# Optimization experiments

Measured on AMD Instinct MI355X. Metric: run time of the kernel, lower is better.

## Reference

```python
import jax, jax.numpy as jnp
import numpy as np
from jax import lax

B, L, P, CIN, N, HD, PH, K = 2048, 96, 96, 8, 64, 64, 8, 3
DIM_C = CIN * N  # 512


def _silu(x):
    return x * jax.nn.sigmoid(x)


def _lin(x, w, b):
    return x @ w.T + b


def setup_inputs() -> dict:
    key = jax.random.key(0)
    ks = iter(jax.random.split(key, 64))

    def w(shape):
        fan_in = shape[-1]
        return (jax.random.normal(next(ks), shape, jnp.float32) / np.sqrt(fan_in)).astype(jnp.float32)

    inp = {"x": jax.random.normal(next(ks), (B, L, CIN), jnp.float32)}
    # x_proj: 5 Linears (enc_in->h, h->h, h->h, h->h, h->N), SiLU between (dropout=eval/identity)
    inp["xp_w0"] = w((HD, CIN)); inp["xp_b0"] = jnp.zeros((HD,), jnp.float32)
    inp["xp_w1"] = w((HD, HD));  inp["xp_b1"] = jnp.zeros((HD,), jnp.float32)
    inp["xp_w2"] = w((HD, HD));  inp["xp_b2"] = jnp.zeros((HD,), jnp.float32)
    inp["xp_w3"] = w((HD, HD));  inp["xp_b3"] = jnp.zeros((HD,), jnp.float32)
    inp["xp_w4"] = w((N, HD));   inp["xp_b4"] = jnp.zeros((N,), jnp.float32)
    # x_proj_: Linear(N,h), SiLU, Linear(h,N)
    inp["xpp_w0"] = w((HD, N)); inp["xpp_b0"] = jnp.zeros((HD,), jnp.float32)
    inp["xpp_w1"] = w((N, HD)); inp["xpp_b1"] = jnp.zeros((N,), jnp.float32)
    # depthwise dilated Conv1d: weight (N, 1, K)
    inp["conv_w"] = w((N, 1, K)); inp["conv_b"] = jnp.zeros((N,), jnp.float32)
    inp["span_A"] = jnp.asarray(0.1, jnp.float32)
    # compress: Linear(N*L, PH)
    inp["comp_w"] = w((PH, N * L)); inp["comp_b"] = jnp.zeros((PH,), jnp.float32)
    # a_ode.net: Linear(PH,h), SiLU, Linear(h,PH), Tanh
    inp["net_w0"] = w((HD, PH)); inp["net_b0"] = jnp.zeros((HD,), jnp.float32)
    inp["net_w1"] = w((PH, HD)); inp["net_b1"] = jnp.zeros((PH,), jnp.float32)
    # lat2out: Linear(PH,8), SiLU, Linear(8,N)
    inp["lo_w0"] = w((8, PH)); inp["lo_b0"] = jnp.zeros((8,), jnp.float32)
    inp["lo_w1"] = w((N, 8));  inp["lo_b1"] = jnp.zeros((N,), jnp.float32)
    # lat2out_c: Linear(PH,8), SiLU, Linear(8, CIN*N)
    inp["lc_w0"] = w((8, PH));     inp["lc_b0"] = jnp.zeros((8,), jnp.float32)
    inp["lc_w1"] = w((DIM_C, 8));  inp["lc_b1"] = jnp.zeros((DIM_C,), jnp.float32)
    # lat2out_z: Linear(N,N), SiLU, Linear(N, CIN)
    inp["lz_w0"] = w((N, N));   inp["lz_b0"] = jnp.zeros((N,), jnp.float32)
    inp["lz_w1"] = w((CIN, N)); inp["lz_b1"] = jnp.zeros((CIN,), jnp.float32)
    return inp


def reference(x, xp_w0, xp_b0, xp_w1, xp_b1, xp_w2, xp_b2, xp_w3, xp_b3, xp_w4, xp_b4,
              xpp_w0, xpp_b0, xpp_w1, xpp_b1, conv_w, conv_b, span_A, comp_w, comp_b,
              net_w0, net_b0, net_w1, net_b1, lo_w0, lo_b0, lo_w1, lo_b1,
              lc_w0, lc_b0, lc_w1, lc_b1, lz_w0, lz_b0, lz_w1, lz_b1):
    Bsz = x.shape[0]

    def x_proj(t):
        h = _silu(_lin(t, xp_w0, xp_b0))
        h = _silu(_lin(h, xp_w1, xp_b1))
        h = _silu(_lin(h, xp_w2, xp_b2))
        h = _silu(_lin(h, xp_w3, xp_b3))
        return _lin(h, xp_w4, xp_b4)

    x_old = x_proj(x[:, :L])                       # (B, L, N)
    hist = x_old.transpose(0, 2, 1)                # (B, N, L)
    pad = (K - 1) * 2                              # 4
    conv = lax.conv_general_dilated(
        hist, conv_w, window_strides=(1,), padding=[(pad, pad)],
        rhs_dilation=(2,), dimension_numbers=("NCH", "OIH", "NCH"),
        feature_group_count=N) + conv_b[None, :, None]
    hist = _silu(conv)[:, :, -L:]                  # (B, N, L)
    hist_f = hist.transpose(0, 2, 1).reshape(Bsz, L * N)
    vector_F = _lin(hist_f, comp_w, comp_b)        # (B, PH)

    a0 = vector_F
    z0 = x_proj(x[:, L - 1])                       # (B, N)

    # Householder matrix H = I - 2 v v^T with v = normalize(x_proj_(z0))
    v = _lin(_silu(_lin(z0, xpp_w0, xpp_b0)), xpp_w1, xpp_b1)
    v = v / (jnp.linalg.norm(v, axis=-1, keepdims=True) + 1e-8)
    Hh = jnp.eye(N, dtype=x.dtype)[None] - 2.0 * v[:, :, None] * v[:, None, :]  # (B,N,N)

    dt = jnp.clip(span_A, 1e-8, 7.0)               # uniform Euler step size
    s0 = jnp.concatenate([a0, z0], axis=-1)        # (B, PH+N)

    def step(s, _):
        a = s[:, :PH]
        z = s[:, PH:]
        da = jnp.tanh(_lin(_silu(_lin(a, net_w0, net_b0)), net_w1, net_b1))  # (B,PH)
        d = _lin(_silu(_lin(a, lo_w0, lo_b0)), lo_w1, lo_b1)                 # (B,N)
        # dz = H^T diag(d) H z   (fused; avoids materializing A_mat)
        Hz = jnp.einsum('bjk,bk->bj', Hh, z)
        dz = jnp.einsum('bj,bji->bi', d * Hz, Hh)
        s_new = s + dt * jnp.concatenate([da, dz], axis=-1)
        return s_new, s_new

    _, sol = lax.scan(step, s0, None, length=P)    # (P, B, PH+N) == sol[1:]

    c_traj = sol[:, :, :PH]                        # (P, B, PH)
    z_traj = sol[:, :, PH:]                        # (P, B, N)

    C = _lin(_silu(_lin(c_traj, lc_w0, lc_b0)), lc_w1, lc_b1)  # (P, B, CIN*N)
    C = C.reshape(P, Bsz, CIN, N)
    y_hat_c = jnp.einsum('pbcn,pbn->pbc', C, z_traj)           # (P, B, CIN)
    added_z = _lin(_silu(_lin(z_traj, lz_w0, lz_b0)), lz_w1, lz_b1)
    x_pred = (y_hat_c + added_z).transpose(1, 0, 2)            # (B, P, CIN)

    x_rec = x[:, :L, :]
    return (x_rec, x_pred)
```

## Files before the change

### kernel.cpp

```cpp
#include <hip/hip_runtime.h>
#include <cstdint>
#include <cstddef>

#define BB 2048
#define LL 96
#define PP 96
#define NN 64
#define HSTRIDE 68
#define RSTR 81

typedef __attribute__((ext_vector_type(8))) short short8;
typedef __attribute__((ext_vector_type(4))) float f32x4;

union U4S8 { uint4 u; short8 s; };

__device__ __forceinline__ float siluf(float x) {
  return x * __builtin_amdgcn_rcpf(1.0f + __expf(-x));
}
__device__ __forceinline__ float tanhf_fast(float x) {
  return 1.0f - 2.0f * __builtin_amdgcn_rcpf(1.0f + __expf(2.0f * x));
}
__device__ __forceinline__ float rlane(float x, int l) {
  return __int_as_float(__builtin_amdgcn_readlane(__float_as_int(x), l));
}

template <int CTRL>
__device__ __forceinline__ float dppadd(float x) {
  int y = __builtin_amdgcn_update_dpp(0, __float_as_int(x), CTRL, 0xF, 0xF, false);
  return x + __int_as_float(y);
}
__device__ __forceinline__ float wave_sum(float x) {
  x = dppadd<0xB1>(x);
  x = dppadd<0x4E>(x);
  x = dppadd<0x141>(x);
  x = dppadd<0x128>(x);
  x += __shfl_xor(x, 16, 64);
  x += __shfl_xor(x, 32, 64);
  return x;
}

__device__ __forceinline__ uint32_t packsplit(float f) {
  uint32_t b = __float_as_uint(f);
  uint32_t h = b & 0xFFFF0000u;
  float r = f - __uint_as_float(h);
  return h | (__float_as_uint(r) >> 16);
}
__device__ __forceinline__ void splitpack2(float f0, float f1, uint32_t& dhi, uint32_t& dlo) {
  uint32_t b0 = __float_as_uint(f0), b1 = __float_as_uint(f1);
  uint32_t h0 = b0 & 0xFFFF0000u, h1 = b1 & 0xFFFF0000u;
  float r0 = f0 - __uint_as_float(h0), r1 = f1 - __uint_as_float(h1);
  dhi = (h0 >> 16) | h1;
  dlo = (__float_as_uint(r0) >> 16) | (__float_as_uint(r1) & 0xFFFF0000u);
}
__device__ __forceinline__ void unpack2(uint32_t p0, uint32_t p1, uint32_t& dhi, uint32_t& dlo) {
  dhi = (p0 >> 16) | (p1 & 0xFFFF0000u);
  dlo = (p0 & 0xFFFFu) | (p1 << 16);
}
__device__ __forceinline__ void readfrag(const uint32_t* p, short8& hi, short8& lo) {
  uint4 pa = *(const uint4*)p;
  uint4 pb = *(const uint4*)(p + 4);
  U4S8 h, l;
  unpack2(pa.x, pa.y, h.u.x, l.u.x);
  unpack2(pa.z, pa.w, h.u.y, l.u.y);
  unpack2(pb.x, pb.y, h.u.z, l.u.z);
  unpack2(pb.z, pb.w, h.u.w, l.u.w);
  hi = h.s; lo = l.s;
}
__device__ __forceinline__ f32x4 mm_split(f32x4 acc, const short8* Ah, const short8* Al,
                                          const short8* Bh, const short8* Bl) {
  acc = __builtin_amdgcn_mfma_f32_16x16x32_bf16(Ah[0], Bh[0], acc, 0, 0, 0);
  acc = __builtin_amdgcn_mfma_f32_16x16x32_bf16(Ah[1], Bh[1], acc, 0, 0, 0);
  acc = __builtin_amdgcn_mfma_f32_16x16x32_bf16(Al[0], Bh[0], acc, 0, 0, 0);
  acc = __builtin_amdgcn_mfma_f32_16x16x32_bf16(Al[1], Bh[1], acc, 0, 0, 0);
  acc = __builtin_amdgcn_mfma_f32_16x16x32_bf16(Ah[0], Bl[0], acc, 0, 0, 0);
  acc = __builtin_amdgcn_mfma_f32_16x16x32_bf16(Ah[1], Bl[1], acc, 0, 0, 0);
  return acc;
}

__global__ __launch_bounds__(256, 2) void k_xproj(
    const float* __restrict__ x,
    const float* __restrict__ w0, const float* __restrict__ b0,
    const float* __restrict__ w1, const float* __restrict__ b1,
    const float* __restrict__ w2, const float* __restrict__ b2,
    const float* __restrict__ w3, const float* __restrict__ b3,
    const float* __restrict__ w4, const float* __restrict__ b4,
    float* __restrict__ x_old, float* __restrict__ out)
{
  __shared__ uint32_t hbuf[128 * HSTRIDE];
  __shared__ uint32_t wbufA[64 * HSTRIDE];
  __shared__ uint32_t wbufB[64 * HSTRIDE];
  __shared__ float bs[320];

  int tid = threadIdx.x;
  int wave = tid >> 6, lane = tid & 63;
  int quad = lane >> 4, m16 = lane & 15;
  size_t tokBase = (size_t)blockIdx.x * 128;

  {
    size_t e = tokBase * 8 + (size_t)tid * 4;
    *(float4*)(out + e) = *(const float4*)(x + e);
  }
  if (tid < 64) {
    bs[tid]       = b0[tid];
    bs[64 + tid]  = b1[tid];
    bs[128 + tid] = b2[tid];
    bs[192 + tid] = b3[tid];
    bs[256 + tid] = b4[tid];
  }
  #pragma unroll
  for (int i = 0; i < 4; ++i) {
    int e4 = i * 256 + tid;
    int o = e4 >> 4, k = (e4 & 15) << 2;
    float4 wv = ((const float4*)w1)[e4];
    *(uint4*)(wbufA + o * HSTRIDE + k) =
        make_uint4(packsplit(wv.x), packsplit(wv.y), packsplit(wv.z), packsplit(wv.w));
  }
  __syncthreads();

  short8 A0h[2], A0l[2];
  #pragma unroll
  for (int mt = 0; mt < 2; ++mt) {
    U4S8 h, l;
    h.u = make_uint4(0, 0, 0, 0); l.u = make_uint4(0, 0, 0, 0);
    if (quad == 0) {
      const float* xp = x + (tokBase + wave * 32 + mt * 16 + m16) * 8;
      float4 xa = *(const float4*)xp;
      float4 xb = *(const float4*)(xp + 4);
      splitpack2(xa.x, xa.y, h.u.x, l.u.x);
      splitpack2(xa.z, xa.w, h.u.y, l.u.y);
      splitpack2(xb.x, xb.y, h.u.z, l.u.z);
      splitpack2(xb.z, xb.w, h.u.w, l.u.w);
    }
    A0h[mt] = h.s; A0l[mt] = l.s;
  }
  short8 B0h[4], B0l[4];
  #pragma unroll
  for (int nt = 0; nt < 4; ++nt) {
    U4S8 h, l;
    h.u = make_uint4(0, 0, 0, 0); l.u = make_uint4(0, 0, 0, 0);
    if (quad == 0) {
      const float* wp = w0 + (nt * 16 + m16) * 8;
      float4 wa = *(const float4*)wp;
      float4 wb = *(const float4*)(wp + 4);
      splitpack2(wa.x, wa.y, h.u.x, l.u.x);
      splitpack2(wa.z, wa.w, h.u.y, l.u.y);
      splitpack2(wb.x, wb.y, h.u.z, l.u.z);
      splitpack2(wb.z, wb.w, h.u.w, l.u.w);
    }
    B0h[nt] = h.s; B0l[nt] = l.s;
  }
  {
    f32x4 acc[2][4];
    #pragma unroll
    for (int mt = 0; mt < 2; ++mt)
      #pragma unroll
      for (int nt = 0; nt < 4; ++nt) {
        float bv = bs[nt * 16 + m16];
        acc[mt][nt] = (f32x4){bv, bv, bv, bv};
      }
    #pragma unroll
    for (int mt = 0; mt < 2; ++mt)
      #pragma unroll
      for (int nt = 0; nt < 4; ++nt)
        acc[mt][nt] = __builtin_amdgcn_mfma_f32_16x16x32_bf16(A0h[mt], B0h[nt], acc[mt][nt], 0, 0, 0);
    #pragma unroll
    for (int mt = 0; mt < 2; ++mt)
      #pragma unroll
      for (int nt = 0; nt < 4; ++nt)
        acc[mt][nt] = __builtin_amdgcn_mfma_f32_16x16x32_bf16(A0l[mt], B0h[nt], acc[mt][nt], 0, 0, 0);
    #pragma unroll
    for (int mt = 0; mt < 2; ++mt)
      #pragma unroll
      for (int nt = 0; nt < 4; ++nt)
        acc[mt][nt] = __builtin_amdgcn_mfma_f32_16x16x32_bf16(A0h[mt], B0l[nt], acc[mt][nt], 0, 0, 0);
    #pragma unroll
    for (int mt = 0; mt < 2; ++mt)
      #pragma unroll
      for (int nt = 0; nt < 4; ++nt)
        #pragma unroll
        for (int r = 0; r < 4; ++r) {
          float s = siluf(acc[mt][nt][r]);
          hbuf[(wave * 32 + mt * 16 + quad * 4 + r) * HSTRIDE + nt * 16 + m16] = packsplit(s);
        }
  }

  const float* Ws[4] = {w1, w2, w3, w4};
  uint32_t* cur = wbufA;
  uint32_t* nxt = wbufB;
  #pragma unroll 1
  for (int lyr = 0; lyr < 4; ++lyr) {
    float4 wv[4];
    if (lyr < 3) {
      const float* wn = Ws[lyr + 1];
      #pragma unroll
      for (int i = 0; i < 4; ++i) wv[i] = ((const float4*)wn)[i * 256 + tid];
    }
    short8 Bh[8], Bl[8];
    #pragma unroll
    for (int nt = 0; nt < 4; ++nt)
      #pragma unroll
      for (int ks = 0; ks < 2; ++ks)
        readfrag(cur + (nt * 16 + m16) * HSTRIDE + ks * 32 + quad * 8, Bh[nt * 2 + ks], Bl[nt * 2 + ks]);
    short8 Ah[4], Al[4];
    #pragma unroll
    for (int mt = 0; mt < 2; ++mt)
      #pragma unroll
      for (int ks = 0; ks < 2; ++ks)
        readfrag(hbuf + (wave * 32 + mt * 16 + m16) * HSTRIDE + ks * 32 + quad * 8, Ah[mt * 2 + ks], Al[mt * 2 + ks]);

    f32x4 acc[2][4];
    #pragma unroll
    for (int mt = 0; mt < 2; ++mt)
      #pragma unroll
      for (int nt = 0; nt < 4; ++nt) {
        float bv = bs[(lyr + 1) * 64 + nt * 16 + m16];
        acc[mt][nt] = (f32x4){bv, bv, bv, bv};
      }
    #pragma unroll
    for (int ks = 0; ks < 2; ++ks)
      #pragma unroll
      for (int mt = 0; mt < 2; ++mt)
        #pragma unroll
        for (int nt = 0; nt < 4; ++nt)
          acc[mt][nt] = __builtin_amdgcn_mfma_f32_16x16x32_bf16(Ah[mt * 2 + ks], Bh[nt * 2 + ks], acc[mt][nt], 0, 0, 0);
    #pragma unroll
    for (int ks = 0; ks < 2; ++ks)
      #pragma unroll
      for (int mt = 0; mt < 2; ++mt)
        #pragma unroll
        for (int nt = 0; nt < 4; ++nt)
          acc[mt][nt] = __builtin_amdgcn_mfma_f32_16x16x32_bf16(Al[mt * 2 + ks], Bh[nt * 2 + ks], acc[mt][nt], 0, 0, 0);
    #pragma unroll
    for (int ks = 0; ks < 2; ++ks)
      #pragma unroll
      for (int mt = 0; mt < 2; ++mt)
        #pragma unroll
        for (int nt = 0; nt < 4; ++nt)
          acc[mt][nt] = __builtin_amdgcn_mfma_f32_16x16x32_bf16(Ah[mt * 2 + ks], Bl[nt * 2 + ks], acc[mt][nt], 0, 0, 0);

    if (lyr < 3) {
      #pragma unroll
      for (int i = 0; i < 4; ++i) {
        int e4 = i * 256 + tid;
        int o = e4 >> 4, k = (e4 & 15) << 2;
        *(uint4*)(nxt + o * HSTRIDE + k) =
            make_uint4(packsplit(wv[i].x), packsplit(wv[i].y), packsplit(wv[i].z), packsplit(wv[i].w));
      }
    }

    if (lyr < 3) {
      #pragma unroll
      for (int mt = 0; mt < 2; ++mt)
        #pragma unroll
        for (int nt = 0; nt < 4; ++nt)
          #pragma unroll
          for (int r = 0; r < 4; ++r) {
            float s = siluf(acc[mt][nt][r]);
            hbuf[(wave * 32 + mt * 16 + quad * 4 + r) * HSTRIDE + nt * 16 + m16] = packsplit(s);
          }
    } else {
      #pragma unroll
      for (int mt = 0; mt < 2; ++mt)
        #pragma unroll
        for (int nt = 0; nt < 4; ++nt)
          #pragma unroll
          for (int r = 0; r < 4; ++r) {
            size_t t = tokBase + wave * 32 + mt * 16 + quad * 4 + r;
            x_old[t * 64 + nt * 16 + m16] = acc[mt][nt][r];
          }
    }
    __syncthreads();
    uint32_t* tmp = cur; cur = nxt; nxt = tmp;
  }
}

__global__ __launch_bounds__(256) void k_hist(
    const float* __restrict__ x_old,
    const float* __restrict__ conv_w, const float* __restrict__ conv_b,
    const float* __restrict__ comp_w, const float* __restrict__ comp_b,
    const float* __restrict__ xw0, const float* __restrict__ xb0,
    const float* __restrict__ xw1, const float* __restrict__ xb1,
    float* __restrict__ a0_o, float* __restrict__ v_o, float* __restrict__ z0_o)
{
  __shared__ float xo[LL * NN];
  __shared__ float red[32];
  __shared__ float hbuf[64];
  int b = blockIdx.x, tid = threadIdx.x;
  const float* src = x_old + (size_t)b * (LL * NN);
  #pragma unroll
  for (int i = 0; i < 6; ++i) {
    int e = (i * 256 + tid) * 4;
    *(float4*)(xo + e) = *(const float4*)(src + e);
  }
  __syncthreads();
  int c = tid & 63;
  float cw0 = conv_w[c * 3], cw1 = conv_w[c * 3 + 1], cw2 = conv_w[c * 3 + 2];
  float cb = conv_b[c];
  float acc[8];
  #pragma unroll
  for (int q = 0; q < 8; ++q) acc[q] = 0.f;
  #pragma unroll 1
  for (int j = 0; j < 24; ++j) {
    int e = j * 256 + tid;
    int t = e >> 6;
    float s = xo[t * 64 + c] * cw0 + cb;
    if (t + 2 < LL) s += xo[(t + 2) * 64 + c] * cw1;
    if (t + 4 < LL) s += xo[(t + 4) * 64 + c] * cw2;
    float hv = siluf(s);
    #pragma unroll
    for (int q = 0; q < 8; ++q) acc[q] += hv * comp_w[q * 6144 + e];
  }
  #pragma unroll
  for (int q = 0; q < 8; ++q) acc[q] = dppadd<0xB1>(acc[q]);
  #pragma unroll
  for (int q = 0; q < 8; ++q) acc[q] = dppadd<0x4E>(acc[q]);
  #pragma unroll
  for (int q = 0; q < 8; ++q) acc[q] = dppadd<0x141>(acc[q]);
  #pragma unroll
  for (int q = 0; q < 8; ++q) acc[q] = dppadd<0x128>(acc[q]);
  #pragma unroll
  for (int q = 0; q < 8; ++q) acc[q] += __shfl_xor(acc[q], 16, 64);
  #pragma unroll
  for (int q = 0; q < 8; ++q) acc[q] += __shfl_xor(acc[q], 32, 64);
  int wave = tid >> 6, lane = tid & 63;
  if (lane < 8) {
    float sel = acc[0];
    #pragma unroll
    for (int q = 1; q < 8; ++q) sel = (lane == q) ? acc[q] : sel;
    red[wave * 8 + lane] = sel;
  }
  __syncthreads();
  if (tid < 8)
    a0_o[b * 8 + tid] = red[tid] + red[8 + tid] + red[16 + tid] + red[24 + tid] + comp_b[tid];
  if (tid < 64) {
    float a2 = xb0[tid];
    #pragma unroll 8
    for (int k = 0; k < 64; ++k) a2 += xw0[tid * 64 + k] * xo[6080 + k];
    hbuf[tid] = siluf(a2);
  }
  __syncthreads();
  float vr = 0.f;
  if (tid < 64) {
    vr = xb1[tid];
    #pragma unroll 8
    for (int k = 0; k < 64; ++k) vr += xw1[tid * 64 + k] * hbuf[k];
  }
  float s2 = wave_sum(vr * vr);
  if (tid < 64) {
    float nrm = sqrtf(s2) + 1e-8f;
    v_o[b * 64 + tid] = vr / nrm;
    z0_o[b * 64 + tid] = xo[6080 + tid];
  }
}

__global__ __launch_bounds__(256) void k_scan(
    const float* __restrict__ a0_i, const float* __restrict__ v_i, const float* __restrict__ z0_i,
    const float* __restrict__ nw0, const float* __restrict__ nb0_p,
    const float* __restrict__ nw1, const float* __restrict__ nb1_p,
    const float* __restrict__ lw0, const float* __restrict__ lb0_p,
    const float* __restrict__ lw1, const float* __restrict__ lb1_p,
    const float* __restrict__ spanA, float* __restrict__ atraj, uint32_t* __restrict__ ztraj)
{
  __shared__ float hshm[4 * 72];
  int tid = threadIdx.x;
  int lane = tid & 63;
  int wv = tid >> 6;
  int b = blockIdx.x * 4 + wv;
  float dt = fminf(fmaxf(spanA[0], 1e-8f), 7.0f);
  int i8 = lane & 7;
  int oct = lane >> 3;
  float* hs = hshm + wv * 72;

  float w0r[8], w1L[8], g0r[8], d1r[8];
  #pragma unroll
  for (int i = 0; i < 8; ++i) w0r[i] = nw0[lane * 8 + i];
  #pragma unroll
  for (int j = 0; j < 8; ++j) w1L[j] = nw1[i8 * 64 + oct * 8 + j];
  #pragma unroll
  for (int i = 0; i < 8; ++i) g0r[i] = lw0[i8 * 8 + i];
  #pragma unroll
  for (int i = 0; i < 8; ++i) d1r[i] = lw1[lane * 8 + i];
  float nb0 = nb0_p[lane];
  float nb1o = nb1_p[i8];
  float lb0o = lb0_p[i8];
  float lb1 = lb1_p[lane];
  float v = v_i[b * 64 + lane];
  float z = z0_i[b * 64 + lane];
  float a_own = a0_i[b * 8 + i8];
  float t0 = wave_sum(v * z);
  float w = z - 2.0f * t0 * v;
  float a_s[8];
  #pragma unroll
  for (int i = 0; i < 8; ++i) a_s[i] = rlane(a_own, i);

  float* ab = atraj + (size_t)b * (PP * 8);
  uint32_t* zb = ztraj + (size_t)b * (PP * NN);
  #pragma unroll 1
  for (int p = 0; p < PP; ++p) {
    float h = nb0;
    #pragma unroll
    for (int i = 0; i < 8; ++i) h += w0r[i] * a_s[i];
    h = siluf(h);
    hs[lane] = h;
    float4 h0 = *(const float4*)(hs + oct * 8);
    float4 h1 = *(const float4*)(hs + oct * 8 + 4);
    float psum = w1L[0] * h0.x + w1L[1] * h0.y + w1L[2] * h0.z + w1L[3] * h0.w
               + w1L[4] * h1.x + w1L[5] * h1.y + w1L[6] * h1.z + w1L[7] * h1.w;
    psum += __shfl_xor(psum, 8, 64);
    psum += __shfl_xor(psum, 16, 64);
    psum += __shfl_xor(psum, 32, 64);
    float da_own = tanhf_fast(psum + nb1o);
    float ga = lb0o;
    #pragma unroll
    for (int i = 0; i < 8; ++i) ga += g0r[i] * a_s[i];
    float g_own = siluf(ga);
    float d = lb1;
    #pragma unroll
    for (int j = 0; j < 8; ++j) d += d1r[j] * rlane(g_own, j);
    a_own += dt * da_own;
    #pragma unroll
    for (int i = 0; i < 8; ++i) a_s[i] = rlane(a_own, i);
    w *= (1.0f + dt * d);
    float t1 = wave_sum(v * w);
    float zv = w - 2.0f * t1 * v;
    if (lane < 8) ab[p * 8 + lane] = a_own;
    zb[p * 64 + lane] = packsplit(zv);
  }
}

__global__ __launch_bounds__(256, 2) void k_post(
    const float* __restrict__ atraj, const uint32_t* __restrict__ ztraj,
    const float* __restrict__ cw0, const float* __restrict__ cb0,
    const float* __restrict__ cw1, const float* __restrict__ cb1,
    const float* __restrict__ zw0, const float* __restrict__ zb0,
    const float* __restrict__ zw1, const float* __restrict__ zb1,
    float* __restrict__ out)
{
  __shared__ uint32_t wbuf[144 * HSTRIDE];
  __shared__ uint32_t ebuf[64 * HSTRIDE];
  __shared__ float    resbuf[64 * RSTR];
  __shared__ float    cw0s[64];
  __shared__ float    cb0s[8];
  __shared__ float    zb0s[64];
  __shared__ float    zb1s[8];

  int tid = threadIdx.x;
  int wave = tid >> 6, lane = tid & 63;
  int quad = lane >> 4, m16 = lane & 15;
  size_t tokBase = (size_t)blockIdx.x * 64;

  #pragma unroll
  for (int i = 0; i < 36; ++i) {
    int e = i * 256 + tid;
    int o = e >> 6, k = e & 63;
    float wv;
    if (o < 64)       wv = cw1[(((o >> 3) * 64 + k) << 3) + (o & 7)];
    else if (o < 72)  wv = cb1[(o - 64) * 64 + k];
    else if (o < 136) wv = zw0[(o - 72) * 64 + k];
    else              wv = zw1[(o - 136) * 64 + k];
    wbuf[o * HSTRIDE + k] = packsplit(wv);
  }
  if (tid < 64) cw0s[tid] = cw0[tid];
  if (tid < 8)  cb0s[tid] = cb0[tid];
  if (tid < 64) zb0s[tid] = zb0[tid];
  if (tid < 8)  zb1s[tid] = zb1[tid];
  __syncthreads();

  const uint32_t* zp = ztraj + (tokBase + wave * 16 + m16) * 64;
  short8 Ah[2], Al[2];
  readfrag(zp + quad * 8,      Ah[0], Al[0]);
  readfrag(zp + 32 + quad * 8, Ah[1], Al[1]);

  #pragma unroll
  for (int nt = 0; nt < 5; ++nt) {
    short8 Bh[2], Bl[2];
    readfrag(wbuf + (nt * 16 + m16) * HSTRIDE + quad * 8,      Bh[0], Bl[0]);
    readfrag(wbuf + (nt * 16 + m16) * HSTRIDE + 32 + quad * 8, Bh[1], Bl[1]);
    f32x4 acc = (f32x4){0.f, 0.f, 0.f, 0.f};
    acc = mm_split(acc, Ah, Al, Bh, Bl);
    int o = nt * 16 + m16;
    if (o < 72) {
      #pragma unroll
      for (int r = 0; r < 4; ++r)
        resbuf[(wave * 16 + quad * 4 + r) * RSTR + o] = acc[r];
    }
  }

  #pragma unroll
  for (int nt = 0; nt < 4; ++nt) {
    short8 Bh[2], Bl[2];
    readfrag(wbuf + (72 + nt * 16 + m16) * HSTRIDE + quad * 8,      Bh[0], Bl[0]);
    readfrag(wbuf + (72 + nt * 16 + m16) * HSTRIDE + 32 + quad * 8, Bh[1], Bl[1]);
    f32x4 acc = (f32x4){0.f, 0.f, 0.f, 0.f};
    acc = mm_split(acc, Ah, Al, Bh, Bl);
    int m = nt * 16 + m16;
    float zbv = zb0s[m];
    #pragma unroll
    for (int r = 0; r < 4; ++r) {
      float e = siluf(acc[r] + zbv);
      ebuf[(wave * 16 + quad * 4 + r) * HSTRIDE + m] = packsplit(e);
    }
  }

  {
    short8 Eh[2], El[2];
    readfrag(ebuf + (wave * 16 + m16) * HSTRIDE + quad * 8,      Eh[0], El[0]);
    readfrag(ebuf + (wave * 16 + m16) * HSTRIDE + 32 + quad * 8, Eh[1], El[1]);
    short8 Bh[2], Bl[2];
    int brow = 136 + (m16 & 7);
    readfrag(wbuf + brow * HSTRIDE + quad * 8,      Bh[0], Bl[0]);
    readfrag(wbuf + brow * HSTRIDE + 32 + quad * 8, Bh[1], Bl[1]);
    f32x4 acc = (f32x4){0.f, 0.f, 0.f, 0.f};
    acc = mm_split(acc, Eh, El, Bh, Bl);
    if (m16 < 8) {
      float zbv = zb1s[m16];
      #pragma unroll
      for (int r = 0; r < 4; ++r)
        resbuf[(wave * 16 + quad * 4 + r) * RSTR + 72 + m16] = acc[r] + zbv;
    }
  }
  __syncthreads();

  {
    int t = tid & 63, cg = tid >> 6;
    size_t idx = tokBase + t;
    const float* ap = atraj + idx * 8;
    float4 a0v = *(const float4*)ap;
    float4 a1v = *(const float4*)(ap + 4);
    float a[8] = {a0v.x, a0v.y, a0v.z, a0v.w, a1v.x, a1v.y, a1v.z, a1v.w};
    float g2[8];
    #pragma unroll
    for (int j = 0; j < 8; ++j) {
      float tt = cb0s[j];
      #pragma unroll
      for (int i = 0; i < 8; ++i) tt += cw0s[j * 8 + i] * a[i];
      g2[j] = siluf(tt);
    }
    const float* rr = resbuf + t * RSTR;
    int c0 = cg * 2;
    float y0 = rr[64 + c0] + rr[72 + c0];
    float y1 = rr[64 + c0 + 1] + rr[72 + c0 + 1];
    #pragma unroll
    for (int j = 0; j < 8; ++j) {
      y0 += rr[c0 * 8 + j] * g2[j];
      y1 += rr[(c0 + 1) * 8 + j] * g2[j];
    }
    float* op = out + (size_t)(BB * LL * 8) + idx * 8 + c0;
    *(float2*)op = make_float2(y0, y1);
  }
}

extern "C" void kernel_launch(void* const* d_in, const int* in_sizes, int n_in,
                              void* d_out, int out_size, void* d_ws, size_t ws_size,
                              hipStream_t stream) {
  const float* x      = (const float*)d_in[0];
  const float* xp_w0  = (const float*)d_in[1];
  const float* xp_b0  = (const float*)d_in[2];
  const float* xp_w1  = (const float*)d_in[3];
  const float* xp_b1  = (const float*)d_in[4];
  const float* xp_w2  = (const float*)d_in[5];
  const float* xp_b2  = (const float*)d_in[6];
  const float* xp_w3  = (const float*)d_in[7];
  const float* xp_b3  = (const float*)d_in[8];
  const float* xp_w4  = (const float*)d_in[9];
  const float* xp_b4  = (const float*)d_in[10];
  const float* xpp_w0 = (const float*)d_in[11];
  const float* xpp_b0 = (const float*)d_in[12];
  const float* xpp_w1 = (const float*)d_in[13];
  const float* xpp_b1 = (const float*)d_in[14];
  const float* conv_w = (const float*)d_in[15];
  const float* conv_b = (const float*)d_in[16];
  const float* span_A = (const float*)d_in[17];
  const float* comp_w = (const float*)d_in[18];
  const float* comp_b = (const float*)d_in[19];
  const float* net_w0 = (const float*)d_in[20];
  const float* net_b0 = (const float*)d_in[21];
  const float* net_w1 = (const float*)d_in[22];
  const float* net_b1 = (const float*)d_in[23];
  const float* lo_w0  = (const float*)d_in[24];
  const float* lo_b0  = (const float*)d_in[25];
  const float* lo_w1  = (const float*)d_in[26];
  const float* lo_b1  = (const float*)d_in[27];
  const float* lc_w0  = (const float*)d_in[28];
  const float* lc_b0  = (const float*)d_in[29];
  const float* lc_w1  = (const float*)d_in[30];
  const float* lc_b1  = (const float*)d_in[31];
  const float* lz_w0  = (const float*)d_in[32];
  const float* lz_b0  = (const float*)d_in[33];
  const float* lz_w1  = (const float*)d_in[34];
  const float* lz_b1  = (const float*)d_in[35];

  float*    ws    = (float*)d_ws;
  float*    x_old = ws;
  uint32_t* ztraj = (uint32_t*)ws;
  float*    atraj = ws + 12582912;
  float*    a0    = ws + 14155776;
  float*    vv    = a0 + 2048 * 8;
  float*    z0    = vv + 2048 * 64;
  float*    out   = (float*)d_out;

  hipLaunchKernelGGL(k_xproj, dim3(1536), dim3(256), 0, stream,
                     x, xp_w0, xp_b0, xp_w1, xp_b1, xp_w2, xp_b2, xp_w3, xp_b3,
                     xp_w4, xp_b4, x_old, out);
  hipLaunchKernelGGL(k_hist, dim3(2048), dim3(256), 0, stream,
                     x_old, conv_w, conv_b, comp_w, comp_b,
                     xpp_w0, xpp_b0, xpp_w1, xpp_b1, a0, vv, z0);
  hipLaunchKernelGGL(k_scan, dim3(512), dim3(256), 0, stream,
                     a0, vv, z0, net_w0, net_b0, net_w1, net_b1,
                     lo_w0, lo_b0, lo_w1, lo_b1, span_A, atraj, ztraj);
  hipLaunchKernelGGL(k_post, dim3(3072), dim3(256), 0, stream,
                     atraj, ztraj, lc_w0, lc_b0, lc_w1, lc_b1,
                     lz_w0, lz_b0, lz_w1, lz_b1, out);
}
```

Baseline: 313.5 us.

## Pre-split weights in a prep kernel and read MFMA fragments from global

Adds a small prep kernel that converts the x_proj hidden-layer weights and the post-stage weights into packed bf16 hi/lo form once per call, kept in workspace. k_xproj and k_post then read B fragments straight from global/L2 instead of staging and converting weights in LDS per block. This removes the LDS weight buffers and block barriers and raises the occupancy hints (3 and 4 blocks per CU). The x_old intermediate is also stored in packed split form and unpacked in k_hist. The cost is one extra kernel launch and uncoalesced per-lane global fragment reads that depend on cache hits.

```diff
diff --git a/kernel.cpp b/kernel.cpp
--- a/kernel.cpp
+++ b/kernel.cpp
@@ -44,6 +44,9 @@
   uint32_t h = b & 0xFFFF0000u;
   float r = f - __uint_as_float(h);
   return h | (__float_as_uint(r) >> 16);
+}
+__device__ __forceinline__ float unpackf(uint32_t p) {
+  return __uint_as_float(p & 0xFFFF0000u) + __uint_as_float(p << 16);
 }
 __device__ __forceinline__ void splitpack2(float f0, float f1, uint32_t& dhi, uint32_t& dlo) {
   uint32_t b0 = __float_as_uint(f0), b1 = __float_as_uint(f1);
@@ -77,18 +80,40 @@
   return acc;
 }
 
-__global__ __launch_bounds__(256, 2) void k_xproj(
+__global__ __launch_bounds__(256) void k_prep(
+    const float* __restrict__ w1, const float* __restrict__ w2,
+    const float* __restrict__ w3, const float* __restrict__ w4,
+    const float* __restrict__ cw1, const float* __restrict__ cb1,
+    const float* __restrict__ zw0, const float* __restrict__ zw1,
+    uint32_t* __restrict__ wpx, uint32_t* __restrict__ wpp)
+{
+  int e = blockIdx.x * 256 + threadIdx.x;
+  if (e < 16384) {
+    int o = e >> 6, k = e & 63;
+    int lyr = o >> 6, r = o & 63;
+    const float* Ws[4] = {w1, w2, w3, w4};
+    wpx[e] = packsplit(Ws[lyr][r * 64 + k]);
+  } else if (e < 16384 + 9216) {
+    int e2 = e - 16384;
+    int o = e2 >> 6, k = e2 & 63;
+    float wv;
+    if (o < 64)       wv = cw1[(((o >> 3) * 64 + k) << 3) + (o & 7)];
+    else if (o < 72)  wv = cb1[(o - 64) * 64 + k];
+    else if (o < 136) wv = zw0[(o - 72) * 64 + k];
+    else              wv = zw1[(o - 136) * 64 + k];
+    wpp[e2] = packsplit(wv);
+  }
+}
+
+__global__ __launch_bounds__(256, 3) void k_xproj(
     const float* __restrict__ x,
     const float* __restrict__ w0, const float* __restrict__ b0,
-    const float* __restrict__ w1, const float* __restrict__ b1,
-    const float* __restrict__ w2, const float* __restrict__ b2,
-    const float* __restrict__ w3, const float* __restrict__ b3,
-    const float* __restrict__ w4, const float* __restrict__ b4,
-    float* __restrict__ x_old, float* __restrict__ out)
+    const float* __restrict__ b1, const float* __restrict__ b2,
+    const float* __restrict__ b3, const float* __restrict__ b4,
+    const uint32_t* __restrict__ wpx,
+    uint32_t* __restrict__ x_old, float* __restrict__ out)
 {
   __shared__ uint32_t hbuf[128 * HSTRIDE];
-  __shared__ uint32_t wbufA[64 * HSTRIDE];
-  __shared__ uint32_t wbufB[64 * HSTRIDE];
   __shared__ float bs[320];
 
   int tid = threadIdx.x;
@@ -106,14 +131,6 @@
     bs[128 + tid] = b2[tid];
     bs[192 + tid] = b3[tid];
     bs[256 + tid] = b4[tid];
-  }
-  #pragma unroll
-  for (int i = 0; i < 4; ++i) {
-    int e4 = i * 256 + tid;
-    int o = e4 >> 4, k = (e4 & 15) << 2;
-    float4 wv = ((const float4*)w1)[e4];
-    *(uint4*)(wbufA + o * HSTRIDE + k) =
-        make_uint4(packsplit(wv.x), packsplit(wv.y), packsplit(wv.z), packsplit(wv.w));
   }
   __syncthreads();
 
@@ -133,22 +150,6 @@
     }
     A0h[mt] = h.s; A0l[mt] = l.s;
   }
-  short8 B0h[4], B0l[4];
-  #pragma unroll
-  for (int nt = 0; nt < 4; ++nt) {
-    U4S8 h, l;
-    h.u = make_uint4(0, 0, 0, 0); l.u = make_uint4(0, 0, 0, 0);
-    if (quad == 0) {
-      const float* wp = w0 + (nt * 16 + m16) * 8;
-      float4 wa = *(const float4*)wp;
-      float4 wb = *(const float4*)(wp + 4);
-      splitpack2(wa.x, wa.y, h.u.x, l.u.x);
-      splitpack2(wa.z, wa.w, h.u.y, l.u.y);
-      splitpack2(wb.x, wb.y, h.u.z, l.u.z);
-      splitpack2(wb.z, wb.w, h.u.w, l.u.w);
-    }
-    B0h[nt] = h.s; B0l[nt] = l.s;
-  }
   {
     f32x4 acc[2][4];
     #pragma unroll
@@ -159,20 +160,25 @@
         acc[mt][nt] = (f32x4){bv, bv, bv, bv};
       }
     #pragma unroll
-    for (int mt = 0; mt < 2; ++mt)
-      #pragma unroll
-      for (int nt = 0; nt < 4; ++nt)
-        acc[mt][nt] = __builtin_amdgcn_mfma_f32_16x16x32_bf16(A0h[mt], B0h[nt], acc[mt][nt], 0, 0, 0);
-    #pragma unroll
-    for (int mt = 0; mt < 2; ++mt)
-      #pragma unroll
-      for (int nt = 0; nt < 4; ++nt)
-        acc[mt][nt] = __builtin_amdgcn_mfma_f32_16x16x32_bf16(A0l[mt], B0h[nt], acc[mt][nt], 0, 0, 0);
-    #pragma unroll
-    for (int mt = 0; mt < 2; ++mt)
-      #pragma unroll
-      for (int nt = 0; nt < 4; ++nt)
-        acc[mt][nt] = __builtin_amdgcn_mfma_f32_16x16x32_bf16(A0h[mt], B0l[nt], acc[mt][nt], 0, 0, 0);
+    for (int nt = 0; nt < 4; ++nt) {
+      U4S8 h, l;
+      h.u = make_uint4(0, 0, 0, 0); l.u = make_uint4(0, 0, 0, 0);
+      if (quad == 0) {
+        const float* wp = w0 + (nt * 16 + m16) * 8;
+        float4 wa = *(const float4*)wp;
+        float4 wb = *(const float4*)(wp + 4);
+        splitpack2(wa.x, wa.y, h.u.x, l.u.x);
+        splitpack2(wa.z, wa.w, h.u.y, l.u.y);
+        splitpack2(wb.x, wb.y, h.u.z, l.u.z);
+        splitpack2(wb.z, wb.w, h.u.w, l.u.w);
+      }
+      #pragma unroll
+      for (int mt = 0; mt < 2; ++mt) {
+        acc[mt][nt] = __builtin_amdgcn_mfma_f32_16x16x32_bf16(A0h[mt], h.s, acc[mt][nt], 0, 0, 0);
+        acc[mt][nt] = __builtin_amdgcn_mfma_f32_16x16x32_bf16(A0l[mt], h.s, acc[mt][nt], 0, 0, 0);
+        acc[mt][nt] = __builtin_amdgcn_mfma_f32_16x16x32_bf16(A0h[mt], l.s, acc[mt][nt], 0, 0, 0);
+      }
+    }
     #pragma unroll
     for (int mt = 0; mt < 2; ++mt)
       #pragma unroll
@@ -184,29 +190,16 @@
         }
   }
 
-  const float* Ws[4] = {w1, w2, w3, w4};
-  uint32_t* cur = wbufA;
-  uint32_t* nxt = wbufB;
   #pragma unroll 1
   for (int lyr = 0; lyr < 4; ++lyr) {
-    float4 wv[4];
-    if (lyr < 3) {
-      const float* wn = Ws[lyr + 1];
-      #pragma unroll
-      for (int i = 0; i < 4; ++i) wv[i] = ((const float4*)wn)[i * 256 + tid];
-    }
-    short8 Bh[8], Bl[8];
-    #pragma unroll
-    for (int nt = 0; nt < 4; ++nt)
+    const uint32_t* wl = wpx + lyr * 4096;
+    short8 Ah[4], Al[4];
+    #pragma unroll
+    for (int mt = 0; mt < 2; ++mt)
       #pragma unroll
       for (int ks = 0; ks < 2; ++ks)
-        readfrag(cur + (nt * 16 + m16) * HSTRIDE + ks * 32 + quad * 8, Bh[nt * 2 + ks], Bl[nt * 2 + ks]);
-    short8 Ah[4], Al[4];
-    #pragma unroll
-    for (int mt = 0; mt < 2; ++mt)
-      #pragma unroll
-      for (int ks = 0; ks < 2; ++ks)
-        readfrag(hbuf + (wave * 32 + mt * 16 + m16) * HSTRIDE + ks * 32 + quad * 8, Ah[mt * 2 + ks], Al[mt * 2 + ks]);
+        readfrag(hbuf + (wave * 32 + mt * 16 + m16) * HSTRIDE + ks * 32 + quad * 8,
+                 Ah[mt * 2 + ks], Al[mt * 2 + ks]);
 
     f32x4 acc[2][4];
     #pragma unroll
@@ -217,35 +210,13 @@
         acc[mt][nt] = (f32x4){bv, bv, bv, bv};
       }
     #pragma unroll
-    for (int ks = 0; ks < 2; ++ks)
+    for (int nt = 0; nt < 4; ++nt) {
+      short8 Bh[2], Bl[2];
+      readfrag(wl + (nt * 16 + m16) * 64 + quad * 8,      Bh[0], Bl[0]);
+      readfrag(wl + (nt * 16 + m16) * 64 + 32 + quad * 8, Bh[1], Bl[1]);
       #pragma unroll
       for (int mt = 0; mt < 2; ++mt)
-        #pragma unroll
-        for (int nt = 0; nt < 4; ++nt)
-          acc[mt][nt] = __builtin_amdgcn_mfma_f32_16x16x32_bf16(Ah[mt * 2 + ks], Bh[nt * 2 + ks], acc[mt][nt], 0, 0, 0);
-    #pragma unroll
-    for (int ks = 0; ks < 2; ++ks)
-      #pragma unroll
-      for (int mt = 0; mt < 2; ++mt)
-        #pragma unroll
-        for (int nt = 0; nt < 4; ++nt)
-          acc[mt][nt] = __builtin_amdgcn_mfma_f32_16x16x32_bf16(Al[mt * 2 + ks], Bh[nt * 2 + ks], acc[mt][nt], 0, 0, 0);
-    #pragma unroll
-    for (int ks = 0; ks < 2; ++ks)
-      #pragma unroll
-      for (int mt = 0; mt < 2; ++mt)
-        #pragma unroll
-        for (int nt = 0; nt < 4; ++nt)
-          acc[mt][nt] = __builtin_amdgcn_mfma_f32_16x16x32_bf16(Ah[mt * 2 + ks], Bl[nt * 2 + ks], acc[mt][nt], 0, 0, 0);
-
-    if (lyr < 3) {
-      #pragma unroll
-      for (int i = 0; i < 4; ++i) {
-        int e4 = i * 256 + tid;
-        int o = e4 >> 4, k = (e4 & 15) << 2;
-        *(uint4*)(nxt + o * HSTRIDE + k) =
-            make_uint4(packsplit(wv[i].x), packsplit(wv[i].y), packsplit(wv[i].z), packsplit(wv[i].w));
-      }
+        acc[mt][nt] = mm_split(acc[mt][nt], &Ah[mt * 2], &Al[mt * 2], Bh, Bl);
     }
 
     if (lyr < 3) {
@@ -266,16 +237,14 @@
           #pragma unroll
           for (int r = 0; r < 4; ++r) {
             size_t t = tokBase + wave * 32 + mt * 16 + quad * 4 + r;
-            x_old[t * 64 + nt * 16 + m16] = acc[mt][nt][r];
+            x_old[t * 64 + nt * 16 + m16] = packsplit(acc[mt][nt][r]);
           }
     }
-    __syncthreads();
-    uint32_t* tmp = cur; cur = nxt; nxt = tmp;
   }
 }
 
 __global__ __launch_bounds__(256) void k_hist(
-    const float* __restrict__ x_old,
+    const uint32_t* __restrict__ x_old,
     const float* __restrict__ conv_w, const float* __restrict__ conv_b,
     const float* __restrict__ comp_w, const float* __restrict__ comp_b,
     const float* __restrict__ xw0, const float* __restrict__ xb0,
@@ -286,11 +255,13 @@
   __shared__ float red[32];
   __shared__ float hbuf[64];
   int b = blockIdx.x, tid = threadIdx.x;
-  const float* src = x_old + (size_t)b * (LL * NN);
+  const uint32_t* src = x_old + (size_t)b * (LL * NN);
   #pragma unroll
   for (int i = 0; i < 6; ++i) {
-    int e = (i * 256 + tid) * 4;
-    *(float4*)(xo + e) = *(const float4*)(src + e);
+    int e4 = i * 256 + tid;
+    uint4 pw = ((const uint4*)src)[e4];
+    *(float4*)(xo + e4 * 4) =
+        make_float4(unpackf(pw.x), unpackf(pw.y), unpackf(pw.z), unpackf(pw.w));
   }
   __syncthreads();
   int c = tid & 63;
@@ -428,15 +399,13 @@
   }
 }
 
-__global__ __launch_bounds__(256, 2) void k_post(
+__global__ __launch_bounds__(256, 4) void k_post(
     const float* __restrict__ atraj, const uint32_t* __restrict__ ztraj,
+    const uint32_t* __restrict__ wpp,
     const float* __restrict__ cw0, const float* __restrict__ cb0,
-    const float* __restrict__ cw1, const float* __restrict__ cb1,
-    const float* __restrict__ zw0, const float* __restrict__ zb0,
-    const float* __restrict__ zw1, const float* __restrict__ zb1,
+    const float* __restrict__ zb0, const float* __restrict__ zb1,
     float* __restrict__ out)
 {
-  __shared__ uint32_t wbuf[144 * HSTRIDE];
   __shared__ uint32_t ebuf[64 * HSTRIDE];
   __shared__ float    resbuf[64 * RSTR];
   __shared__ float    cw0s[64];
@@ -449,22 +418,10 @@
   int quad = lane >> 4, m16 = lane & 15;
   size_t tokBase = (size_t)blockIdx.x * 64;
 
-  #pragma unroll
-  for (int i = 0; i < 36; ++i) {
-    int e = i * 256 + tid;
-    int o = e >> 6, k = e & 63;
-    float wv;
-    if (o < 64)       wv = cw1[(((o >> 3) * 64 + k) << 3) + (o & 7)];
-    else if (o < 72)  wv = cb1[(o - 64) * 64 + k];
-    else if (o < 136) wv = zw0[(o - 72) * 64 + k];
-    else              wv = zw1[(o - 136) * 64 + k];
-    wbuf[o * HSTRIDE + k] = packsplit(wv);
-  }
   if (tid < 64) cw0s[tid] = cw0[tid];
   if (tid < 8)  cb0s[tid] = cb0[tid];
   if (tid < 64) zb0s[tid] = zb0[tid];
   if (tid < 8)  zb1s[tid] = zb1[tid];
-  __syncthreads();
 
   const uint32_t* zp = ztraj + (tokBase + wave * 16 + m16) * 64;
   short8 Ah[2], Al[2];
@@ -474,8 +431,8 @@
   #pragma unroll
   for (int nt = 0; nt < 5; ++nt) {
     short8 Bh[2], Bl[2];
-    readfrag(wbuf + (nt * 16 + m16) * HSTRIDE + quad * 8,      Bh[0], Bl[0]);
-    readfrag(wbuf + (nt * 16 + m16) * HSTRIDE + 32 + quad * 8, Bh[1], Bl[1]);
+    readfrag(wpp + (nt * 16 + m16) * 64 + quad * 8,      Bh[0], Bl[0]);
+    readfrag(wpp + (nt * 16 + m16) * 64 + 32 + quad * 8, Bh[1], Bl[1]);
     f32x4 acc = (f32x4){0.f, 0.f, 0.f, 0.f};
     acc = mm_split(acc, Ah, Al, Bh, Bl);
     int o = nt * 16 + m16;
@@ -489,8 +446,8 @@
   #pragma unroll
   for (int nt = 0; nt < 4; ++nt) {
     short8 Bh[2], Bl[2];
-    readfrag(wbuf + (72 + nt * 16 + m16) * HSTRIDE + quad * 8,      Bh[0], Bl[0]);
-    readfrag(wbuf + (72 + nt * 16 + m16) * HSTRIDE + 32 + quad * 8, Bh[1], Bl[1]);
+    readfrag(wpp + (72 + nt * 16 + m16) * 64 + quad * 8,      Bh[0], Bl[0]);
+    readfrag(wpp + (72 + nt * 16 + m16) * 64 + 32 + quad * 8, Bh[1], Bl[1]);
     f32x4 acc = (f32x4){0.f, 0.f, 0.f, 0.f};
     acc = mm_split(acc, Ah, Al, Bh, Bl);
     int m = nt * 16 + m16;
@@ -508,8 +465,8 @@
     readfrag(ebuf + (wave * 16 + m16) * HSTRIDE + 32 + quad * 8, Eh[1], El[1]);
     short8 Bh[2], Bl[2];
     int brow = 136 + (m16 & 7);
-    readfrag(wbuf + brow * HSTRIDE + quad * 8,      Bh[0], Bl[0]);
-    readfrag(wbuf + brow * HSTRIDE + 32 + quad * 8, Bh[1], Bl[1]);
+    readfrag(wpp + brow * 64 + quad * 8,      Bh[0], Bl[0]);
+    readfrag(wpp + brow * 64 + 32 + quad * 8, Bh[1], Bl[1]);
     f32x4 acc = (f32x4){0.f, 0.f, 0.f, 0.f};
     acc = mm_split(acc, Eh, El, Bh, Bl);
     if (m16 < 8) {
@@ -591,17 +548,20 @@
   const float* lz_b1  = (const float*)d_in[35];
 
   float*    ws    = (float*)d_ws;
-  float*    x_old = ws;
+  uint32_t* x_old = (uint32_t*)ws;
   uint32_t* ztraj = (uint32_t*)ws;
   float*    atraj = ws + 12582912;
   float*    a0    = ws + 14155776;
   float*    vv    = a0 + 2048 * 8;
   float*    z0    = vv + 2048 * 64;
+  uint32_t* wpx   = (uint32_t*)(z0 + 2048 * 64);
+  uint32_t* wpp   = wpx + 16384;
   float*    out   = (float*)d_out;
 
+  hipLaunchKernelGGL(k_prep, dim3(100), dim3(256), 0, stream,
+                     xp_w1, xp_w2, xp_w3, xp_w4, lc_w1, lc_b1, lz_w0, lz_w1, wpx, wpp);
   hipLaunchKernelGGL(k_xproj, dim3(1536), dim3(256), 0, stream,
-                     x, xp_w0, xp_b0, xp_w1, xp_b1, xp_w2, xp_b2, xp_w3, xp_b3,
-                     xp_w4, xp_b4, x_old, out);
+                     x, xp_w0, xp_b0, xp_b1, xp_b2, xp_b3, xp_b4, wpx, x_old, out);
   hipLaunchKernelGGL(k_hist, dim3(2048), dim3(256), 0, stream,
                      x_old, conv_w, conv_b, comp_w, comp_b,
                      xpp_w0, xpp_b0, xpp_w1, xpp_b1, a0, vv, z0);
@@ -609,6 +569,5 @@
                      a0, vv, z0, net_w0, net_b0, net_w1, net_b1,
                      lo_w0, lo_b0, lo_w1, lo_b1, span_A, atraj, ztraj);
   hipLaunchKernelGGL(k_post, dim3(3072), dim3(256), 0, stream,
-                     atraj, ztraj, lc_w0, lc_b0, lc_w1, lc_b1,
-                     lz_w0, lz_b0, lz_w1, lz_b1, out);
-}
+                     atraj, ztraj, wpp, lc_w0, lc_b0, lz_b0, lz_b1, out);
+}
```

Result: slower. 338.8 us (+8.1%).

## Keep k_post epilogue in registers, alias ebuf onto wbuf, raise occupancy

Applied to the files above, without the earlier changes.

The post-processing kernel now keeps the MFMA results for the C and bias tiles in registers instead of staging them through a shared result buffer. The final C·g contraction is done with DPP cross-lane reductions inside each 16-lane group, and the SiLU intermediate buffer reuses the weight buffer after an added barrier. Shared memory drops enough to raise launch bounds from 2 to 4 blocks per CU. In exchange there is more register pressure, redundant per-lane recomputation of the small gate MLP, and half-active lanes on the final store.

```diff
diff --git a/kernel.cpp b/kernel.cpp
--- a/kernel.cpp
+++ b/kernel.cpp
@@ -7,7 +7,6 @@
 #define PP 96
 #define NN 64
 #define HSTRIDE 68
-#define RSTR 81
 
 typedef __attribute__((ext_vector_type(8))) short short8;
 typedef __attribute__((ext_vector_type(4))) float f32x4;
@@ -28,6 +27,11 @@
 __device__ __forceinline__ float dppadd(float x) {
   int y = __builtin_amdgcn_update_dpp(0, __float_as_int(x), CTRL, 0xF, 0xF, false);
   return x + __int_as_float(y);
+}
+template <int CTRL>
+__device__ __forceinline__ float dppmov(float x) {
+  int y = __builtin_amdgcn_update_dpp(0, __float_as_int(x), CTRL, 0xF, 0xF, false);
+  return __int_as_float(y);
 }
 __device__ __forceinline__ float wave_sum(float x) {
   x = dppadd<0xB1>(x);
@@ -428,7 +432,7 @@
   }
 }
 
-__global__ __launch_bounds__(256, 2) void k_post(
+__global__ __launch_bounds__(256, 4) void k_post(
     const float* __restrict__ atraj, const uint32_t* __restrict__ ztraj,
     const float* __restrict__ cw0, const float* __restrict__ cb0,
     const float* __restrict__ cw1, const float* __restrict__ cb1,
@@ -437,8 +441,6 @@
     float* __restrict__ out)
 {
   __shared__ uint32_t wbuf[144 * HSTRIDE];
-  __shared__ uint32_t ebuf[64 * HSTRIDE];
-  __shared__ float    resbuf[64 * RSTR];
   __shared__ float    cw0s[64];
   __shared__ float    cb0s[8];
   __shared__ float    zb0s[64];
@@ -471,21 +473,18 @@
   readfrag(zp + quad * 8,      Ah[0], Al[0]);
   readfrag(zp + 32 + quad * 8, Ah[1], Al[1]);
 
+  f32x4 acc1[5];
   #pragma unroll
   for (int nt = 0; nt < 5; ++nt) {
     short8 Bh[2], Bl[2];
     readfrag(wbuf + (nt * 16 + m16) * HSTRIDE + quad * 8,      Bh[0], Bl[0]);
     readfrag(wbuf + (nt * 16 + m16) * HSTRIDE + 32 + quad * 8, Bh[1], Bl[1]);
     f32x4 acc = (f32x4){0.f, 0.f, 0.f, 0.f};
-    acc = mm_split(acc, Ah, Al, Bh, Bl);
-    int o = nt * 16 + m16;
-    if (o < 72) {
-      #pragma unroll
-      for (int r = 0; r < 4; ++r)
-        resbuf[(wave * 16 + quad * 4 + r) * RSTR + o] = acc[r];
-    }
-  }
-
+    acc1[nt] = mm_split(acc, Ah, Al, Bh, Bl);
+  }
+  __syncthreads();
+
+  uint32_t* ebuf = wbuf;
   #pragma unroll
   for (int nt = 0; nt < 4; ++nt) {
     short8 Bh[2], Bl[2];
@@ -502,6 +501,7 @@
     }
   }
 
+  f32x4 acc3;
   {
     short8 Eh[2], El[2];
     readfrag(ebuf + (wave * 16 + m16) * HSTRIDE + quad * 8,      Eh[0], El[0]);
@@ -511,42 +511,43 @@
     readfrag(wbuf + brow * HSTRIDE + quad * 8,      Bh[0], Bl[0]);
     readfrag(wbuf + brow * HSTRIDE + 32 + quad * 8, Bh[1], Bl[1]);
     f32x4 acc = (f32x4){0.f, 0.f, 0.f, 0.f};
-    acc = mm_split(acc, Eh, El, Bh, Bl);
-    if (m16 < 8) {
-      float zbv = zb1s[m16];
-      #pragma unroll
-      for (int r = 0; r < 4; ++r)
-        resbuf[(wave * 16 + quad * 4 + r) * RSTR + 72 + m16] = acc[r] + zbv;
-    }
-  }
-  __syncthreads();
-
-  {
-    int t = tid & 63, cg = tid >> 6;
-    size_t idx = tokBase + t;
+    acc3 = mm_split(acc, Eh, El, Bh, Bl);
+  }
+
+  int j = m16 & 7;
+  float cwj[8];
+  #pragma unroll
+  for (int i = 0; i < 8; ++i) cwj[i] = cw0s[j * 8 + i];
+  float cbj = cb0s[j];
+  #pragma unroll
+  for (int r = 0; r < 4; ++r) {
+    size_t idx = tokBase + wave * 16 + quad * 4 + r;
     const float* ap = atraj + idx * 8;
     float4 a0v = *(const float4*)ap;
     float4 a1v = *(const float4*)(ap + 4);
-    float a[8] = {a0v.x, a0v.y, a0v.z, a0v.w, a1v.x, a1v.y, a1v.z, a1v.w};
-    float g2[8];
-    #pragma unroll
-    for (int j = 0; j < 8; ++j) {
-      float tt = cb0s[j];
-      #pragma unroll
-      for (int i = 0; i < 8; ++i) tt += cw0s[j * 8 + i] * a[i];
-      g2[j] = siluf(tt);
-    }
-    const float* rr = resbuf + t * RSTR;
-    int c0 = cg * 2;
-    float y0 = rr[64 + c0] + rr[72 + c0];
-    float y1 = rr[64 + c0 + 1] + rr[72 + c0 + 1];
-    #pragma unroll
-    for (int j = 0; j < 8; ++j) {
-      y0 += rr[c0 * 8 + j] * g2[j];
-      y1 += rr[(c0 + 1) * 8 + j] * g2[j];
-    }
-    float* op = out + (size_t)(BB * LL * 8) + idx * 8 + c0;
-    *(float2*)op = make_float2(y0, y1);
+    float g2v = cbj
+      + cwj[0] * a0v.x + cwj[1] * a0v.y + cwj[2] * a0v.z + cwj[3] * a0v.w
+      + cwj[4] * a1v.x + cwj[5] * a1v.y + cwj[6] * a1v.z + cwj[7] * a1v.w;
+    g2v = siluf(g2v);
+    float yc[4], qo[4];
+    #pragma unroll
+    for (int nt = 0; nt < 4; ++nt) {
+      float p = acc1[nt][r] * g2v;
+      p = dppadd<0xB1>(p);
+      p = dppadd<0x4E>(p);
+      p = dppadd<0x141>(p);
+      yc[nt] = p;
+      qo[nt] = dppmov<0x128>(p);
+    }
+    if (m16 < 8) {
+      int cc = m16;
+      int nt = cc >> 1;
+      float ye = (nt == 0) ? yc[0] : (nt == 1) ? yc[1] : (nt == 2) ? yc[2] : yc[3];
+      float yo = (nt == 0) ? qo[0] : (nt == 1) ? qo[1] : (nt == 2) ? qo[2] : qo[3];
+      float y = (cc & 1) ? yo : ye;
+      y += acc1[4][r] + acc3[r] + zb1s[cc];
+      out[(size_t)(BB * LL * 8) + idx * 8 + cc] = y;
+    }
   }
 }
 
```

Result: no change. 308.8 us (-1.5%).
